# Performance work log

Hardware: AMD Instinct MI355X
Metric: run time of the kernel (lower is better)

Reference implementation:

```python
import jax, jax.numpy as jnp
import numpy as np

B, K, G, C = 64, 4000, 200, 91
LAMBDA_BOX, LAMBDA_CLS, LAMBDA_OBJ = 5.0, 1.0, 1.0
EPS = 1e-9


def _make_boxes(key, lead_shape):
    k1, k2 = jax.random.split(key)
    tl = jax.random.uniform(k1, lead_shape + (2,)) * 0.7
    wh = jax.random.uniform(k2, lead_shape + (2,)) * 0.29 + 0.01
    return jnp.concatenate([tl, tl + wh], axis=-1)


def setup_inputs() -> dict:
    key = jax.random.key(0)
    ks = jax.random.split(key, 6)
    pred_boxes = _make_boxes(ks[0], (B, K))
    pred_obj_logits = jax.random.normal(ks[1], (B, K), dtype=jnp.float32)
    pred_cls_logits = jax.random.normal(ks[2], (B, K, C), dtype=jnp.float32)
    gt_boxes = _make_boxes(ks[3], (B, G))
    gt_labels = jax.random.randint(ks[4], (B, G), 0, C)
    n_gt = jax.random.randint(ks[5], (B,), 1, G + 1)
    gt_mask = jnp.arange(G)[None, :] < n_gt[:, None]
    return dict(pred_boxes=pred_boxes, pred_obj_logits=pred_obj_logits,
                pred_cls_logits=pred_cls_logits, gt_boxes=gt_boxes,
                gt_labels=gt_labels, gt_mask=gt_mask)


def _area(x):
    return jnp.clip(x[..., 2] - x[..., 0], 0.0) * jnp.clip(x[..., 3] - x[..., 1], 0.0)


def _pairwise_iou(a, b):
    # a: (K,4), b: (G,4) -> (K,G)
    tl = jnp.maximum(a[:, None, :2], b[None, :, :2])
    br = jnp.minimum(a[:, None, 2:], b[None, :, 2:])
    wh = jnp.clip(br - tl, 0.0)
    inter = wh[..., 0] * wh[..., 1]
    union = jnp.clip(_area(a)[:, None] + _area(b)[None, :] - inter, EPS)
    return inter / union


def _ciou_loss(pb, gb):
    # pb, gb: (M,4) matched pairs; elementwise CIoU loss = 1 - CIoU
    tl = jnp.maximum(pb[:, :2], gb[:, :2])
    br = jnp.minimum(pb[:, 2:], gb[:, 2:])
    wh = jnp.clip(br - tl, 0.0)
    inter = wh[:, 0] * wh[:, 1]
    iou = inter / jnp.clip(_area(pb) + _area(gb) - inter, EPS)
    px = (pb[:, 0] + pb[:, 2]) * 0.5
    py = (pb[:, 1] + pb[:, 3]) * 0.5
    tx = (gb[:, 0] + gb[:, 2]) * 0.5
    ty = (gb[:, 1] + gb[:, 3]) * 0.5
    rho2 = (px - tx) ** 2 + (py - ty) ** 2
    etl = jnp.minimum(pb[:, :2], gb[:, :2])
    ebr = jnp.maximum(pb[:, 2:], gb[:, 2:])
    c2 = jnp.clip((ebr[:, 0] - etl[:, 0]) ** 2 + (ebr[:, 1] - etl[:, 1]) ** 2, EPS)
    pw = jnp.clip(pb[:, 2] - pb[:, 0], EPS)
    ph = jnp.clip(pb[:, 3] - pb[:, 1], EPS)
    tw = jnp.clip(gb[:, 2] - gb[:, 0], EPS)
    th = jnp.clip(gb[:, 3] - gb[:, 1], EPS)
    v = (4.0 / jnp.pi ** 2) * (jnp.arctan(tw / th) - jnp.arctan(pw / ph)) ** 2
    alpha = jax.lax.stop_gradient(v / (1.0 - iou + v + EPS))  # torch.no_grad
    return 1.0 - (iou - rho2 / c2 - alpha * v)


def _greedy_match(iou0):
    # iou0: (K,G), invalid gt columns pre-masked to -1. Fixed min(K,G)-step
    # argmax-and-mask scan reproducing the torch greedy loop (break -> valid=False).
    Gd = iou0.shape[1]
    steps = min(iou0.shape[0], Gd)

    def step(m, _):
        flat = jnp.argmax(m)
        p = flat // Gd
        g = flat % Gd
        valid = m.reshape(-1)[flat] >= 0.0
        m2 = m.at[p, :].set(-1.0).at[:, g].set(-1.0)
        return jnp.where(valid, m2, m), (p, g, valid)

    _, (ps, gs, vs) = jax.lax.scan(step, iou0, None, length=steps)
    return ps, gs, vs


def _per_batch(pred_b, cls_b, gt_b, labels_b, mask_b):
    iou = jax.lax.stop_gradient(_pairwise_iou(pred_b, gt_b))  # matching is non-diff (.item() in torch)
    iou = jnp.where(mask_b[None, :], iou, -1.0)
    ps, gs, vs = _greedy_match(iou)
    vf = vs.astype(pred_b.dtype)
    n = jnp.sum(vf)
    denom = jnp.maximum(n, 1.0)
    pb = pred_b[ps]
    gb = gt_b[gs]
    lbox = jnp.sum(_ciou_loss(pb, gb) * vf) / denom
    logp = jax.nn.log_softmax(cls_b[ps], axis=-1)
    lce = -jnp.take_along_axis(logp, labels_b[gs][:, None], axis=1)[:, 0]
    lcls = jnp.sum(lce * vf) / denom
    obj_tgt = jnp.zeros((pred_b.shape[0],), pred_b.dtype).at[
        jnp.where(vs, ps, pred_b.shape[0])].set(1.0, mode='drop')
    return lbox, lcls, obj_tgt, n > 0.0


def reference(pred_boxes, pred_obj_logits, pred_cls_logits, gt_boxes, gt_labels, gt_mask):
    lbox_b, lcls_b, obj_tgt, has = jax.vmap(_per_batch)(
        pred_boxes, pred_cls_logits, gt_boxes, gt_labels, gt_mask)
    hf = has.astype(pred_boxes.dtype)
    nb = jnp.maximum(jnp.sum(hf), 1.0)
    loss_box = jnp.sum(lbox_b * hf) / nb
    loss_cls = jnp.sum(lcls_b * hf) / nb
    # BCEWithLogits(mean): softplus(x) - t*x
    loss_obj = jnp.mean(jax.nn.softplus(pred_obj_logits) - obj_tgt * pred_obj_logits)
    total = LAMBDA_BOX * loss_box + LAMBDA_CLS * loss_cls + LAMBDA_OBJ * loss_obj
    return total, loss_box, loss_cls, loss_obj
```

## Files before the change

### kernel.cpp

```cpp
#include <hip/hip_runtime.h>
#include <math.h>

#define B_ 64
#define K_ 4000
#define G_ 200
#define C_ 91
#define EPS_ 1e-9f
#define NW_ 16
typedef unsigned long long ull;

#define WS_FLAG 0
#define WS_PART 256
#define WS_CNT 1536
#define WS_MATCH 2048
#define WS_ROWUSED 53248
#define WS_TOP 327680

__device__ __forceinline__ float box_area(float4 a) {
#pragma clang fp contract(off)
  return fmaxf(a.z - a.x, 0.f) * fmaxf(a.w - a.y, 0.f);
}

__device__ __forceinline__ float iou_ab(float4 a, float aA, float4 b, float aB) {
#pragma clang fp contract(off)
  float tlx = fmaxf(a.x, b.x), tly = fmaxf(a.y, b.y);
  float brx = fminf(a.z, b.z), bry = fminf(a.w, b.w);
  float w = fmaxf(brx - tlx, 0.f), h = fmaxf(bry - tly, 0.f);
  float inter = w * h;
  float uni = fmaxf(aA + aB - inter, EPS_);
  return inter / uni;
}

__device__ __forceinline__ float ciou_loss(float4 p, float4 g) {
  float tlx = fmaxf(p.x, g.x), tly = fmaxf(p.y, g.y);
  float brx = fminf(p.z, g.z), bry = fminf(p.w, g.w);
  float w = fmaxf(brx - tlx, 0.f), h = fmaxf(bry - tly, 0.f);
  float inter = w * h;
  float areaP = fmaxf(p.z - p.x, 0.f) * fmaxf(p.w - p.y, 0.f);
  float areaG = fmaxf(g.z - g.x, 0.f) * fmaxf(g.w - g.y, 0.f);
  float iou = inter / fmaxf(areaP + areaG - inter, EPS_);
  float px = (p.x + p.z) * 0.5f, py = (p.y + p.w) * 0.5f;
  float tx = (g.x + g.z) * 0.5f, ty = (g.y + g.w) * 0.5f;
  float rho2 = (px - tx) * (px - tx) + (py - ty) * (py - ty);
  float ex = fmaxf(p.z, g.z) - fminf(p.x, g.x);
  float ey = fmaxf(p.w, g.w) - fminf(p.y, g.y);
  float c2 = fmaxf(ex * ex + ey * ey, EPS_);
  float pw = fmaxf(p.z - p.x, EPS_), ph = fmaxf(p.w - p.y, EPS_);
  float tw = fmaxf(g.z - g.x, EPS_), th = fmaxf(g.w - g.y, EPS_);
  float dat = atanf(tw / th) - atanf(pw / ph);
  float v = (4.0f / (float)(M_PI * M_PI)) * dat * dat;
  float alpha = v / ((1.f - iou) + v + EPS_);
  return 1.f - (iou - rho2 / c2 - alpha * v);
}

__global__ void kdetect(const unsigned char* m8, int* flag) {
  int b = threadIdx.x;
  int ok = 1;
  const unsigned char* r = m8 + b * G_;
  if (r[0] != 1) ok = 0;
  int seen0 = 0;
  for (int g = 0; g < G_; ++g) {
    unsigned char c = r[g];
    if (c > 1) { ok = 0; break; }
    if (c == 0) seen0 = 1;
    else if (seen0) { ok = 0; break; }
  }
  int all = __all(ok);
  if (b == 0) *flag = all ? 1 : 0;
}

__device__ __forceinline__ float block_sum(float v, float* s_red) {
  for (int off = 32; off > 0; off >>= 1) v += __shfl_xor(v, off);
  int lane = threadIdx.x & 63, wid = threadIdx.x >> 6;
  if (lane == 0) s_red[wid] = v;
  __syncthreads();
  float r = 0.f;
  if (wid == 0) {
    float t = (lane < NW_) ? s_red[lane] : 0.f;
    for (int off = 32; off > 0; off >>= 1) t += __shfl_xor(t, off);
    r = t;
  }
  __syncthreads();
  return r;
}

__device__ __forceinline__ ull wave_maxkey(ull k) {
  for (int off = 32; off > 0; off >>= 1) {
    ull o = __shfl_xor(k, off);
    if (o > k) k = o;
  }
  return k;
}

#define TOP8_INS(key)                                   \
  if ((key) > t7) {                                     \
    t7 = (key);                                         \
    ull tmp_;                                           \
    if (t7 > t6) { tmp_ = t6; t6 = t7; t7 = tmp_; }     \
    if (t6 > t5) { tmp_ = t5; t5 = t6; t6 = tmp_; }     \
    if (t5 > t4) { tmp_ = t4; t4 = t5; t5 = tmp_; }     \
    if (t4 > t3) { tmp_ = t3; t3 = t4; t4 = tmp_; }     \
    if (t3 > t2) { tmp_ = t2; t2 = t3; t3 = tmp_; }     \
    if (t2 > t1) { tmp_ = t1; t1 = t2; t2 = tmp_; }     \
    if (t1 > t0) { tmp_ = t0; t0 = t1; t1 = tmp_; }     \
  }

__device__ __forceinline__ void merge8(ull* __restrict__ d, ull* __restrict__ x,
                                       ull* __restrict__ y) {
#pragma unroll
  for (int o = 0; o < 8; ++o) {
    bool tx = x[0] >= y[0];
    d[o] = tx ? x[0] : y[0];
#pragma unroll
    for (int q = 0; q < 7; ++q) {
      ull nx = x[q + 1], ny = y[q + 1];
      x[q] = tx ? nx : x[q];
      y[q] = tx ? y[q] : ny;
    }
    x[7] = tx ? 0ull : x[7];
    y[7] = tx ? y[7] : 0ull;
  }
}

__global__ __launch_bounds__(1024) void kinit(const float* __restrict__ pred_boxes,
                                              const float* __restrict__ gt_boxes,
                                              const void* __restrict__ gt_mask,
                                              char* __restrict__ ws) {
  __shared__ float s_gx[G_], s_gy[G_], s_gz[G_], s_gw[G_], s_garea[G_];
  __shared__ unsigned char s_valid[G_];
  __shared__ ull s_mbuf[64][5][8];
  const int b = blockIdx.x >> 2, sl = blockIdx.x & 3;
  const int tid = threadIdx.x;
  const int msk8 = *(const int*)(ws + WS_FLAG);
  const float4* p4 = (const float4*)pred_boxes + (size_t)b * K_;
  const float4* g4 = (const float4*)gt_boxes + (size_t)b * G_;

  for (int g = tid; g < G_; g += 1024) {
    float4 gb = g4[g];
    s_gx[g] = gb.x; s_gy[g] = gb.y; s_gz[g] = gb.z; s_gw[g] = gb.w;
    s_garea[g] = box_area(gb);
    int v;
    if (msk8) v = ((const unsigned char*)gt_mask)[(size_t)b * G_ + g] != 0;
    else      v = ((const int*)gt_mask)[(size_t)b * G_ + g] != 0;
    s_valid[g] = (unsigned char)v;
  }
  __syncthreads();

  const int c = tid / 5, j = tid - 5 * c;
  const bool active = (tid < 1000) && s_valid[c];
  ull t0 = 0, t1 = 0, t2 = 0, t3 = 0, t4 = 0, t5 = 0, t6 = 0, t7 = 0;
  if (active) {
    float4 gb = make_float4(s_gx[c], s_gy[c], s_gz[c], s_gw[c]);
    float gA = s_garea[c];
    const int k0 = sl * 1000 + j * 200;
    for (int i = 0; i < 200; ++i) {
      int k = k0 + i;
      float4 pb = p4[k];
      float iou = iou_ab(pb, box_area(pb), gb, gA);
      ull e = ((ull)__float_as_uint(iou) << 12) | (ull)(4095 - k);
      TOP8_INS(e);
    }
  }
  ull* wtop = (ull*)(ws + WS_TOP) + (size_t)(b * 4 + sl) * G_ * 8;
  for (int r = 0; r < 4; ++r) {
    int rc = c - 64 * r;
    if (active && rc >= 0 && rc < 64) {
      s_mbuf[rc][j][0] = t0; s_mbuf[rc][j][1] = t1;
      s_mbuf[rc][j][2] = t2; s_mbuf[rc][j][3] = t3;
      s_mbuf[rc][j][4] = t4; s_mbuf[rc][j][5] = t5;
      s_mbuf[rc][j][6] = t6; s_mbuf[rc][j][7] = t7;
    }
    __syncthreads();
    if (tid < 64) {
      int cc = 64 * r + tid;
      if (cc < G_) {
        if (s_valid[cc]) {
          int i0 = 0, i1 = 0, i2 = 0, i3 = 0, i4 = 0;
          for (int o = 0; o < 8; ++o) {
            ull v0 = (i0 < 8) ? s_mbuf[tid][0][i0] : 0ull;
            ull v1 = (i1 < 8) ? s_mbuf[tid][1][i1] : 0ull;
            ull v2 = (i2 < 8) ? s_mbuf[tid][2][i2] : 0ull;
            ull v3 = (i3 < 8) ? s_mbuf[tid][3][i3] : 0ull;
            ull v4 = (i4 < 8) ? s_mbuf[tid][4][i4] : 0ull;
            ull best = v0; int jb = 0;
            if (v1 > best) { best = v1; jb = 1; }
            if (v2 > best) { best = v2; jb = 2; }
            if (v3 > best) { best = v3; jb = 3; }
            if (v4 > best) { best = v4; jb = 4; }
            if (jb == 0) ++i0; else if (jb == 1) ++i1; else if (jb == 2) ++i2;
            else if (jb == 3) ++i3; else ++i4;
            wtop[cc * 8 + o] = best;
          }
        } else {
          for (int o = 0; o < 8; ++o) wtop[cc * 8 + o] = 0ull;
        }
      }
    }
    __syncthreads();
  }
}

__global__ __launch_bounds__(64) void kmatch(const float* __restrict__ pred_boxes,
                                             const float* __restrict__ gt_boxes,
                                             char* __restrict__ ws) {
  __shared__ float s_gx[G_], s_gy[G_], s_gz[G_], s_gw[G_], s_garea[G_];
  __shared__ unsigned char s_rowused[K_];
  __shared__ ull s_toplist[G_][8];
  __shared__ int s_mp[G_];
  __shared__ unsigned short s_mg[G_];
  const int b = blockIdx.x;
  const int lane = threadIdx.x;
  const float4* p4 = (const float4*)pred_boxes + (size_t)b * K_;
  const float4* g4 = (const float4*)gt_boxes + (size_t)b * G_;

  for (int g = lane; g < G_; g += 64) {
    float4 gb = g4[g];
    s_gx[g] = gb.x; s_gy[g] = gb.y; s_gz[g] = gb.z; s_gw[g] = gb.w;
    s_garea[g] = box_area(gb);
  }
  for (int k = lane; k < K_; k += 64) s_rowused[k] = 0;

  const ull* wtop = (const ull*)(ws + WS_TOP);
  ull key0 = 0, key1 = 0, key2 = 0, key3 = 0;
  int ptr0 = 8, ptr1 = 8, ptr2 = 8, ptr3 = 8;
  int cloc = 0;
#define SLOTLOAD(S)                                                        \
  { int col = S * 64 + lane;                                               \
    if (col < G_) {                                                        \
      ull La[8], Lb[8], M1[8], M2[8], Mf[8];                               \
      _Pragma("unroll") for (int o = 0; o < 8; ++o)                        \
        La[o] = wtop[((size_t)(b * 4 + 0) * G_ + col) * 8 + o];            \
      _Pragma("unroll") for (int o = 0; o < 8; ++o)                        \
        Lb[o] = wtop[((size_t)(b * 4 + 1) * G_ + col) * 8 + o];            \
      merge8(M1, La, Lb);                                                  \
      _Pragma("unroll") for (int o = 0; o < 8; ++o)                        \
        La[o] = wtop[((size_t)(b * 4 + 2) * G_ + col) * 8 + o];            \
      _Pragma("unroll") for (int o = 0; o < 8; ++o)                        \
        Lb[o] = wtop[((size_t)(b * 4 + 3) * G_ + col) * 8 + o];            \
      merge8(M2, La, Lb);                                                  \
      merge8(Mf, M1, M2);                                                  \
      _Pragma("unroll") for (int o = 0; o < 8; ++o) s_toplist[col][o] = Mf[o]; \
      if (Mf[0] != 0ull) {                                                 \
        key##S = (Mf[0] << 8) | (ull)(255 - col); ptr##S = 1; ++cloc; } } }
  SLOTLOAD(0) SLOTLOAD(1) SLOTLOAD(2) SLOTLOAD(3)
#undef SLOTLOAD
  for (int off = 32; off > 0; off >>= 1) cloc += __shfl_xor(cloc, off);
  const int cnt = cloc;

  for (int step = 0; step < cnt;) {
    ull a1 = key0, a2 = key1;
    if (key1 > key0) { a1 = key1; a2 = key0; }
    if (key2 > a1) { a2 = a1; a1 = key2; } else if (key2 > a2) a2 = key2;
    if (key3 > a1) { a2 = a1; a1 = key3; } else if (key3 > a2) a2 = key3;
    for (int off = 32; off > 0; off >>= 1) {
      ull b1 = __shfl_xor(a1, off), b2 = __shfl_xor(a2, off);
      if (b1 > a1) { a2 = (a1 > b2) ? a1 : b2; a1 = b1; }
      else { a2 = (b1 > a2) ? b1 : a2; }
    }
    const int p1 = 4095 - (int)((a1 >> 8) & 0xFFF);
    const int g1v = 255 - (int)(a1 & 0xFF);
    const int p2 = 4095 - (int)((a2 >> 8) & 0xFFF);
    const int g2v = 255 - (int)(a2 & 0xFF);
    const bool do2 = (a2 != 0ull) && (p2 != p1) && (step + 1 < cnt);
    if (lane == 0) {
      s_mp[step] = p1; s_mg[step] = (unsigned short)g1v; s_rowused[p1] = 1;
      if (do2) { s_mp[step + 1] = p2; s_mg[step + 1] = (unsigned short)g2v; s_rowused[p2] = 1; }
    }
    __builtin_amdgcn_wave_barrier();
    const int gd2 = do2 ? g2v : -1;
    const int pd2 = do2 ? p2 : -1;
    int need = 0;
#define DEMOTE(S)                                                          \
    { int col = S * 64 + lane; ull kk = key##S;                            \
      if (kk != 0ull) {                                                    \
        if (col == g1v || col == gd2) { key##S = 0ull; }                   \
        else { int krow = 4095 - (int)((kk >> 8) & 0xFFF);                 \
          if (krow == p1 || krow == pd2) {                                 \
            ull nk = 0ull; int np = ptr##S;                                \
            while (np < 8) {                                               \
              ull e = s_toplist[col][np]; ++np;                            \
              int pr = 4095 - (int)((e >> 12) & 0xFFF);                    \
              if (e != 0ull && !s_rowused[pr]) {                           \
                nk = (e << 8) | (ull)(255 - col); break; } }               \
            ptr##S = np; key##S = nk;                                      \
            if (nk == 0ull) need |= (1 << S); } } } }
    DEMOTE(0) DEMOTE(1) DEMOTE(2) DEMOTE(3)
#undef DEMOTE
    while (__any(need)) {
      unsigned long long bal = __ballot(need != 0);
      int src = (int)__builtin_ctzll(bal);
      int myslot = need ? __builtin_ctz(need) : 0;
      int slot = __shfl(myslot, src);
      int col = slot * 64 + src;
      float4 gb = make_float4(s_gx[col], s_gy[col], s_gz[col], s_gw[col]);
      float gA = s_garea[col];
      ull r1 = 0ull, r2 = 0ull;
      for (int k = lane; k < K_; k += 64) {
        if (!s_rowused[k]) {
          float4 pb = p4[k];
          float iou = iou_ab(pb, box_area(pb), gb, gA);
          ull e = ((ull)__float_as_uint(iou) << 12) | (ull)(4095 - k);
          if (e > r1) { r2 = r1; r1 = e; }
          else if (e > r2) r2 = e;
        }
      }
      ull m1 = wave_maxkey(r1);
      ull cnd = (r1 == m1) ? r2 : r1;
      ull m2 = wave_maxkey(cnd);
      if (lane == src) {
        ull nk = (m1 << 8) | (ull)(255 - col);
        if (slot == 0) key0 = nk; else if (slot == 1) key1 = nk;
        else if (slot == 2) key2 = nk; else key3 = nk;
        int npv = m2 ? 7 : 8;
        if (m2) s_toplist[col][7] = m2;
        if (slot == 0) ptr0 = npv; else if (slot == 1) ptr1 = npv;
        else if (slot == 2) ptr2 = npv; else ptr3 = npv;
        need &= ~(1 << slot);
      }
    }
    step += do2 ? 2 : 1;
  }

  unsigned* mout = (unsigned*)(ws + WS_MATCH) + b * G_;
  for (int i = lane; i < cnt; i += 64)
    mout[i] = ((unsigned)s_mp[i] << 8) | (unsigned)s_mg[i];
  unsigned* ruo = (unsigned*)(ws + WS_ROWUSED + (size_t)b * K_);
  const unsigned* rus = (const unsigned*)s_rowused;
  for (int i = lane; i < K_ / 4; i += 64) ruo[i] = rus[i];
  if (lane == 0) ((int*)(ws + WS_CNT))[b] = cnt;
}

__global__ __launch_bounds__(1024) void kepi(const float* __restrict__ pred_boxes,
                                             const float* __restrict__ obj_logits,
                                             const float* __restrict__ cls_logits,
                                             const float* __restrict__ gt_boxes,
                                             const int* __restrict__ gt_labels,
                                             char* __restrict__ ws) {
  __shared__ float s_red[NW_];
  const int b = blockIdx.x;
  const int tid = threadIdx.x;
  const int cnt = ((const int*)(ws + WS_CNT))[b];
  const unsigned* mm = (const unsigned*)(ws + WS_MATCH) + b * G_;
  const unsigned char* ru = (const unsigned char*)(ws + WS_ROWUSED) + (size_t)b * K_;
  const float4* p4 = (const float4*)pred_boxes + (size_t)b * K_;
  const float4* g4 = (const float4*)gt_boxes + (size_t)b * G_;

  float lbox = 0.f, lcls = 0.f;
  for (int i = tid; i < cnt; i += 1024) {
    unsigned e = mm[i];
    int p = (int)(e >> 8), g = (int)(e & 0xFF);
    float4 pb = p4[p];
    float4 gb = g4[g];
    lbox += ciou_loss(pb, gb);
    int label = gt_labels[(size_t)b * G_ + g];
    const float* lg = cls_logits + ((size_t)b * K_ + p) * C_;
    float m = -1e30f;
    for (int cc = 0; cc < C_; ++cc) m = fmaxf(m, lg[cc]);
    float s = 0.f;
    for (int cc = 0; cc < C_; ++cc) s += expf(lg[cc] - m);
    lcls += (m + logf(s)) - lg[label];
  }
  float obj = 0.f;
  const float* ol = obj_logits + (size_t)b * K_;
  for (int k = tid; k < K_; k += 1024) {
    float x = ol[k];
    float sp = fmaxf(x, 0.f) + log1pf(expf(-fabsf(x)));
    if (ru[k]) sp -= x;
    obj += sp;
  }
  lbox = block_sum(lbox, s_red);
  lcls = block_sum(lcls, s_red);
  obj = block_sum(obj, s_red);
  if (tid == 0) {
    float* partials = (float*)(ws + WS_PART);
    float n = (float)cnt;
    float denom = fmaxf(n, 1.f);
    partials[b * 4 + 0] = lbox / denom;
    partials[b * 4 + 1] = lcls / denom;
    partials[b * 4 + 2] = obj;
    partials[b * 4 + 3] = (n > 0.f) ? 1.f : 0.f;
  }
}

__global__ void kfinal(const char* __restrict__ ws, float* __restrict__ out) {
  int b = threadIdx.x;
  const float* partials = (const float*)(ws + WS_PART);
  float lb = partials[b * 4 + 0], lc = partials[b * 4 + 1];
  float ob = partials[b * 4 + 2], hf = partials[b * 4 + 3];
  float sb = lb * hf, sc = lc * hf, sh = hf, so = ob;
  for (int off = 32; off > 0; off >>= 1) {
    sb += __shfl_xor(sb, off);
    sc += __shfl_xor(sc, off);
    sh += __shfl_xor(sh, off);
    so += __shfl_xor(so, off);
  }
  if (b == 0) {
    float nb = fmaxf(sh, 1.f);
    float box = sb / nb, cls = sc / nb;
    float obj = so / (float)(B_ * K_);
    out[0] = 5.f * box + cls + obj;
    out[1] = box;
    out[2] = cls;
    out[3] = obj;
  }
}

extern "C" void kernel_launch(void* const* d_in, const int* in_sizes, int n_in,
                              void* d_out, int out_size, void* d_ws, size_t ws_size,
                              hipStream_t stream) {
  const float* pred_boxes = (const float*)d_in[0];
  const float* obj_logits = (const float*)d_in[1];
  const float* cls_logits = (const float*)d_in[2];
  const float* gt_boxes = (const float*)d_in[3];
  const int* gt_labels = (const int*)d_in[4];
  const void* gt_mask = d_in[5];
  float* out = (float*)d_out;
  char* ws = (char*)d_ws;

  hipLaunchKernelGGL(kdetect, dim3(1), dim3(64), 0, stream,
                     (const unsigned char*)gt_mask, (int*)(ws + WS_FLAG));
  hipLaunchKernelGGL(kinit, dim3(B_ * 4), dim3(1024), 0, stream,
                     pred_boxes, gt_boxes, gt_mask, ws);
  hipLaunchKernelGGL(kmatch, dim3(B_), dim3(64), 0, stream,
                     pred_boxes, gt_boxes, ws);
  hipLaunchKernelGGL(kepi, dim3(B_), dim3(1024), 0, stream,
                     pred_boxes, obj_logits, cls_logits, gt_boxes, gt_labels, ws);
  hipLaunchKernelGGL(kfinal, dim3(1), dim3(64), 0, stream, ws, out);
}
```

Before: 304.8 us.

## Keep top-16 IoU candidates per GT column to reduce full rescans in matching

The per-column candidate list grows from 8 to 16 entries, and the prediction axis is now split across 2 blocks per batch instead of 4, with each thread scanning 400 predictions. The serial greedy matcher merges two 16-lists instead of four 8-lists. It also looks up two candidates per iteration in the demotion loop, padding the row-used array to 4096 so the speculative read stays in bounds. The goal is to cut the costly single-wave full rescans of all K rows when a column's list runs out. In exchange, the init kernel has half as many blocks, does twice the work per thread and keeps a 16-deep insertion sort in registers.

```diff
diff --git a/kernel.cpp b/kernel.cpp
--- a/kernel.cpp
+++ b/kernel.cpp
@@ -92,33 +92,41 @@
   return k;
 }
 
-#define TOP8_INS(key)                                   \
-  if ((key) > t7) {                                     \
-    t7 = (key);                                         \
-    ull tmp_;                                           \
-    if (t7 > t6) { tmp_ = t6; t6 = t7; t7 = tmp_; }     \
-    if (t6 > t5) { tmp_ = t5; t5 = t6; t6 = tmp_; }     \
-    if (t5 > t4) { tmp_ = t4; t4 = t5; t5 = tmp_; }     \
-    if (t4 > t3) { tmp_ = t3; t3 = t4; t4 = tmp_; }     \
-    if (t3 > t2) { tmp_ = t2; t2 = t3; t3 = tmp_; }     \
-    if (t2 > t1) { tmp_ = t1; t1 = t2; t2 = tmp_; }     \
-    if (t1 > t0) { tmp_ = t0; t0 = t1; t1 = tmp_; }     \
-  }
-
-__device__ __forceinline__ void merge8(ull* __restrict__ d, ull* __restrict__ x,
-                                       ull* __restrict__ y) {
+#define TOP16_INS(key)                                    \
+  if ((key) > t15) {                                      \
+    t15 = (key);                                          \
+    ull tmp_;                                             \
+    if (t15 > t14) { tmp_ = t14; t14 = t15; t15 = tmp_; } \
+    if (t14 > t13) { tmp_ = t13; t13 = t14; t14 = tmp_; } \
+    if (t13 > t12) { tmp_ = t12; t12 = t13; t13 = tmp_; } \
+    if (t12 > t11) { tmp_ = t11; t11 = t12; t12 = tmp_; } \
+    if (t11 > t10) { tmp_ = t10; t10 = t11; t11 = tmp_; } \
+    if (t10 > t9)  { tmp_ = t9;  t9 = t10;  t10 = tmp_; } \
+    if (t9 > t8)   { tmp_ = t8;  t8 = t9;   t9 = tmp_; }  \
+    if (t8 > t7)   { tmp_ = t7;  t7 = t8;   t8 = tmp_; }  \
+    if (t7 > t6)   { tmp_ = t6;  t6 = t7;   t7 = tmp_; }  \
+    if (t6 > t5)   { tmp_ = t5;  t5 = t6;   t6 = tmp_; }  \
+    if (t5 > t4)   { tmp_ = t4;  t4 = t5;   t5 = tmp_; }  \
+    if (t4 > t3)   { tmp_ = t3;  t3 = t4;   t4 = tmp_; }  \
+    if (t3 > t2)   { tmp_ = t2;  t2 = t3;   t3 = tmp_; }  \
+    if (t2 > t1)   { tmp_ = t1;  t1 = t2;   t2 = tmp_; }  \
+    if (t1 > t0)   { tmp_ = t0;  t0 = t1;   t1 = tmp_; }  \
+  }
+
+__device__ __forceinline__ void merge16(ull* __restrict__ d, ull* __restrict__ x,
+                                        ull* __restrict__ y) {
 #pragma unroll
-  for (int o = 0; o < 8; ++o) {
+  for (int o = 0; o < 16; ++o) {
     bool tx = x[0] >= y[0];
     d[o] = tx ? x[0] : y[0];
 #pragma unroll
-    for (int q = 0; q < 7; ++q) {
+    for (int q = 0; q < 15; ++q) {
       ull nx = x[q + 1], ny = y[q + 1];
       x[q] = tx ? nx : x[q];
       y[q] = tx ? y[q] : ny;
     }
-    x[7] = tx ? 0ull : x[7];
-    y[7] = tx ? y[7] : 0ull;
+    x[15] = tx ? 0ull : x[15];
+    y[15] = tx ? y[15] : 0ull;
   }
 }
 
@@ -128,8 +136,8 @@
                                               char* __restrict__ ws) {
   __shared__ float s_gx[G_], s_gy[G_], s_gz[G_], s_gw[G_], s_garea[G_];
   __shared__ unsigned char s_valid[G_];
-  __shared__ ull s_mbuf[64][5][8];
-  const int b = blockIdx.x >> 2, sl = blockIdx.x & 3;
+  __shared__ ull s_mbuf[64][5][16];
+  const int b = blockIdx.x >> 1, sl = blockIdx.x & 1;
   const int tid = threadIdx.x;
   const int msk8 = *(const int*)(ws + WS_FLAG);
   const float4* p4 = (const float4*)pred_boxes + (size_t)b * K_;
@@ -149,26 +157,31 @@
   const int c = tid / 5, j = tid - 5 * c;
   const bool active = (tid < 1000) && s_valid[c];
   ull t0 = 0, t1 = 0, t2 = 0, t3 = 0, t4 = 0, t5 = 0, t6 = 0, t7 = 0;
+  ull t8 = 0, t9 = 0, t10 = 0, t11 = 0, t12 = 0, t13 = 0, t14 = 0, t15 = 0;
   if (active) {
     float4 gb = make_float4(s_gx[c], s_gy[c], s_gz[c], s_gw[c]);
     float gA = s_garea[c];
-    const int k0 = sl * 1000 + j * 200;
-    for (int i = 0; i < 200; ++i) {
+    const int k0 = sl * 2000 + j * 400;
+    for (int i = 0; i < 400; ++i) {
       int k = k0 + i;
       float4 pb = p4[k];
       float iou = iou_ab(pb, box_area(pb), gb, gA);
       ull e = ((ull)__float_as_uint(iou) << 12) | (ull)(4095 - k);
-      TOP8_INS(e);
-    }
-  }
-  ull* wtop = (ull*)(ws + WS_TOP) + (size_t)(b * 4 + sl) * G_ * 8;
+      TOP16_INS(e);
+    }
+  }
+  ull* wtop = (ull*)(ws + WS_TOP) + (size_t)(b * 2 + sl) * G_ * 16;
   for (int r = 0; r < 4; ++r) {
     int rc = c - 64 * r;
     if (active && rc >= 0 && rc < 64) {
-      s_mbuf[rc][j][0] = t0; s_mbuf[rc][j][1] = t1;
-      s_mbuf[rc][j][2] = t2; s_mbuf[rc][j][3] = t3;
-      s_mbuf[rc][j][4] = t4; s_mbuf[rc][j][5] = t5;
-      s_mbuf[rc][j][6] = t6; s_mbuf[rc][j][7] = t7;
+      s_mbuf[rc][j][0] = t0;   s_mbuf[rc][j][1] = t1;
+      s_mbuf[rc][j][2] = t2;   s_mbuf[rc][j][3] = t3;
+      s_mbuf[rc][j][4] = t4;   s_mbuf[rc][j][5] = t5;
+      s_mbuf[rc][j][6] = t6;   s_mbuf[rc][j][7] = t7;
+      s_mbuf[rc][j][8] = t8;   s_mbuf[rc][j][9] = t9;
+      s_mbuf[rc][j][10] = t10; s_mbuf[rc][j][11] = t11;
+      s_mbuf[rc][j][12] = t12; s_mbuf[rc][j][13] = t13;
+      s_mbuf[rc][j][14] = t14; s_mbuf[rc][j][15] = t15;
     }
     __syncthreads();
     if (tid < 64) {
@@ -176,12 +189,12 @@
       if (cc < G_) {
         if (s_valid[cc]) {
           int i0 = 0, i1 = 0, i2 = 0, i3 = 0, i4 = 0;
-          for (int o = 0; o < 8; ++o) {
-            ull v0 = (i0 < 8) ? s_mbuf[tid][0][i0] : 0ull;
-            ull v1 = (i1 < 8) ? s_mbuf[tid][1][i1] : 0ull;
-            ull v2 = (i2 < 8) ? s_mbuf[tid][2][i2] : 0ull;
-            ull v3 = (i3 < 8) ? s_mbuf[tid][3][i3] : 0ull;
-            ull v4 = (i4 < 8) ? s_mbuf[tid][4][i4] : 0ull;
+          for (int o = 0; o < 16; ++o) {
+            ull v0 = (i0 < 16) ? s_mbuf[tid][0][i0] : 0ull;
+            ull v1 = (i1 < 16) ? s_mbuf[tid][1][i1] : 0ull;
+            ull v2 = (i2 < 16) ? s_mbuf[tid][2][i2] : 0ull;
+            ull v3 = (i3 < 16) ? s_mbuf[tid][3][i3] : 0ull;
+            ull v4 = (i4 < 16) ? s_mbuf[tid][4][i4] : 0ull;
             ull best = v0; int jb = 0;
             if (v1 > best) { best = v1; jb = 1; }
             if (v2 > best) { best = v2; jb = 2; }
@@ -189,10 +202,10 @@
             if (v4 > best) { best = v4; jb = 4; }
             if (jb == 0) ++i0; else if (jb == 1) ++i1; else if (jb == 2) ++i2;
             else if (jb == 3) ++i3; else ++i4;
-            wtop[cc * 8 + o] = best;
+            wtop[cc * 16 + o] = best;
           }
         } else {
-          for (int o = 0; o < 8; ++o) wtop[cc * 8 + o] = 0ull;
+          for (int o = 0; o < 16; ++o) wtop[cc * 16 + o] = 0ull;
         }
       }
     }
@@ -204,8 +217,8 @@
                                              const float* __restrict__ gt_boxes,
                                              char* __restrict__ ws) {
   __shared__ float s_gx[G_], s_gy[G_], s_gz[G_], s_gw[G_], s_garea[G_];
-  __shared__ unsigned char s_rowused[K_];
-  __shared__ ull s_toplist[G_][8];
+  __shared__ unsigned char s_rowused[4096];
+  __shared__ ull s_toplist[G_][16];
   __shared__ int s_mp[G_];
   __shared__ unsigned short s_mg[G_];
   const int b = blockIdx.x;
@@ -218,29 +231,23 @@
     s_gx[g] = gb.x; s_gy[g] = gb.y; s_gz[g] = gb.z; s_gw[g] = gb.w;
     s_garea[g] = box_area(gb);
   }
-  for (int k = lane; k < K_; k += 64) s_rowused[k] = 0;
+  for (int k = lane; k < 4096; k += 64) s_rowused[k] = 0;
 
   const ull* wtop = (const ull*)(ws + WS_TOP);
   ull key0 = 0, key1 = 0, key2 = 0, key3 = 0;
-  int ptr0 = 8, ptr1 = 8, ptr2 = 8, ptr3 = 8;
+  int ptr0 = 16, ptr1 = 16, ptr2 = 16, ptr3 = 16;
   int cloc = 0;
-#define SLOTLOAD(S)                                                        \
-  { int col = S * 64 + lane;                                               \
-    if (col < G_) {                                                        \
-      ull La[8], Lb[8], M1[8], M2[8], Mf[8];                               \
-      _Pragma("unroll") for (int o = 0; o < 8; ++o)                        \
-        La[o] = wtop[((size_t)(b * 4 + 0) * G_ + col) * 8 + o];            \
-      _Pragma("unroll") for (int o = 0; o < 8; ++o)                        \
-        Lb[o] = wtop[((size_t)(b * 4 + 1) * G_ + col) * 8 + o];            \
-      merge8(M1, La, Lb);                                                  \
-      _Pragma("unroll") for (int o = 0; o < 8; ++o)                        \
-        La[o] = wtop[((size_t)(b * 4 + 2) * G_ + col) * 8 + o];            \
-      _Pragma("unroll") for (int o = 0; o < 8; ++o)                        \
-        Lb[o] = wtop[((size_t)(b * 4 + 3) * G_ + col) * 8 + o];            \
-      merge8(M2, La, Lb);                                                  \
-      merge8(Mf, M1, M2);                                                  \
-      _Pragma("unroll") for (int o = 0; o < 8; ++o) s_toplist[col][o] = Mf[o]; \
-      if (Mf[0] != 0ull) {                                                 \
+#define SLOTLOAD(S)                                                         \
+  { int col = S * 64 + lane;                                                \
+    if (col < G_) {                                                         \
+      ull La[16], Lb[16], Mf[16];                                           \
+      _Pragma("unroll") for (int o = 0; o < 16; ++o)                        \
+        La[o] = wtop[((size_t)(b * 2 + 0) * G_ + col) * 16 + o];            \
+      _Pragma("unroll") for (int o = 0; o < 16; ++o)                        \
+        Lb[o] = wtop[((size_t)(b * 2 + 1) * G_ + col) * 16 + o];            \
+      merge16(Mf, La, Lb);                                                  \
+      _Pragma("unroll") for (int o = 0; o < 16; ++o) s_toplist[col][o] = Mf[o]; \
+      if (Mf[0] != 0ull) {                                                  \
         key##S = (Mf[0] << 8) | (ull)(255 - col); ptr##S = 1; ++cloc; } } }
   SLOTLOAD(0) SLOTLOAD(1) SLOTLOAD(2) SLOTLOAD(3)
 #undef SLOTLOAD
@@ -270,19 +277,27 @@
     const int gd2 = do2 ? g2v : -1;
     const int pd2 = do2 ? p2 : -1;
     int need = 0;
-#define DEMOTE(S)                                                          \
-    { int col = S * 64 + lane; ull kk = key##S;                            \
-      if (kk != 0ull) {                                                    \
-        if (col == g1v || col == gd2) { key##S = 0ull; }                   \
-        else { int krow = 4095 - (int)((kk >> 8) & 0xFFF);                 \
-          if (krow == p1 || krow == pd2) {                                 \
-            ull nk = 0ull; int np = ptr##S;                                \
-            while (np < 8) {                                               \
-              ull e = s_toplist[col][np]; ++np;                            \
-              int pr = 4095 - (int)((e >> 12) & 0xFFF);                    \
-              if (e != 0ull && !s_rowused[pr]) {                           \
-                nk = (e << 8) | (ull)(255 - col); break; } }               \
-            ptr##S = np; key##S = nk;                                      \
+#define DEMOTE(S)                                                           \
+    { int col = S * 64 + lane; ull kk = key##S;                             \
+      if (kk != 0ull) {                                                     \
+        if (col == g1v || col == gd2) { key##S = 0ull; }                    \
+        else { int krow = 4095 - (int)((kk >> 8) & 0xFFF);                  \
+          if (krow == p1 || krow == pd2) {                                  \
+            ull nk = 0ull; int np = ptr##S;                                 \
+            while (np < 16) {                                               \
+              ull e0 = s_toplist[col][np];                                  \
+              ull e1 = (np + 1 < 16) ? s_toplist[col][np + 1] : 0ull;       \
+              int pr0 = 4095 - (int)((e0 >> 12) & 0xFFF);                   \
+              int pr1 = 4095 - (int)((e1 >> 12) & 0xFFF);                   \
+              unsigned char u0 = s_rowused[pr0];                            \
+              unsigned char u1 = s_rowused[pr1];                            \
+              if (e0 == 0ull) { np = 16; break; }                           \
+              if (!u0) { nk = (e0 << 8) | (ull)(255 - col); np += 1; break; } \
+              if (e1 == 0ull) { np = 16; break; }                           \
+              if (!u1) { nk = (e1 << 8) | (ull)(255 - col); np += 2; break; } \
+              np += 2;                                                      \
+            }                                                               \
+            ptr##S = np; key##S = nk;                                       \
             if (nk == 0ull) need |= (1 << S); } } } }
     DEMOTE(0) DEMOTE(1) DEMOTE(2) DEMOTE(3)
 #undef DEMOTE
@@ -311,8 +326,8 @@
         ull nk = (m1 << 8) | (ull)(255 - col);
         if (slot == 0) key0 = nk; else if (slot == 1) key1 = nk;
         else if (slot == 2) key2 = nk; else key3 = nk;
-        int npv = m2 ? 7 : 8;
-        if (m2) s_toplist[col][7] = m2;
+        int npv = m2 ? 15 : 16;
+        if (m2) s_toplist[col][15] = m2;
         if (slot == 0) ptr0 = npv; else if (slot == 1) ptr1 = npv;
         else if (slot == 2) ptr2 = npv; else ptr3 = npv;
         need &= ~(1 << slot);
@@ -419,7 +434,7 @@
 
   hipLaunchKernelGGL(kdetect, dim3(1), dim3(64), 0, stream,
                      (const unsigned char*)gt_mask, (int*)(ws + WS_FLAG));
-  hipLaunchKernelGGL(kinit, dim3(B_ * 4), dim3(1024), 0, stream,
+  hipLaunchKernelGGL(kinit, dim3(B_ * 2), dim3(1024), 0, stream,
                      pred_boxes, gt_boxes, gt_mask, ws);
   hipLaunchKernelGGL(kmatch, dim3(B_), dim3(64), 0, stream,
                      pred_boxes, gt_boxes, ws);
```

After: 684.0 us. 2.24x slower.
